# Kernel tuning notes

Measured on AMD Instinct MI355X. Metric: run time of the kernel, lower is better.

The kernel has to match this reference:

```python
import jax, jax.numpy as jnp
import numpy as np

DIM = 2048
N_HEADS = 32
N_KV_HEADS = 8
HEAD_DIM = 64
N_REP = N_HEADS // N_KV_HEADS
SEQ = 2048
BATCH = 1


def _llama3_scaled_rope(head_dim, end, base=10000.0, scale_factor=8):
    # matches executorch precompute_freqs_cis with use_scaled=True
    freqs = 1.0 / (base ** (np.arange(0, head_dim, 2)[: head_dim // 2] / head_dim))
    low_freq_factor, high_freq_factor, old_ctx = 1.0, 4.0, 8192.0
    low_wl = old_ctx / low_freq_factor
    high_wl = old_ctx / high_freq_factor
    wavelen = 2.0 * np.pi / freqs
    smooth = (old_ctx / wavelen - low_freq_factor) / (high_freq_factor - low_freq_factor)
    scaled = np.where(
        wavelen < high_wl,
        freqs,
        np.where(wavelen > low_wl, freqs / scale_factor,
                 (1.0 - smooth) * freqs / scale_factor + smooth * freqs),
    )
    t = np.arange(end, dtype=np.float64)
    ang = np.outer(t, scaled)
    return np.cos(ang).astype(np.float32), np.sin(ang).astype(np.float32)


def setup_inputs() -> dict:
    key = jax.random.key(0)
    kx, kq, kk, kv, ko = jax.random.split(key, 5)
    x = jax.random.normal(kx, (BATCH, SEQ, DIM), dtype=jnp.float32)
    sc = 0.02
    wq = jax.random.normal(kq, (N_HEADS * HEAD_DIM, DIM), dtype=jnp.float32) * sc
    wk = jax.random.normal(kk, (N_KV_HEADS * HEAD_DIM, DIM), dtype=jnp.float32) * sc
    wv = jax.random.normal(kv, (N_KV_HEADS * HEAD_DIM, DIM), dtype=jnp.float32) * sc
    wo = jax.random.normal(ko, (N_HEADS * HEAD_DIM, DIM), dtype=jnp.float32).T * sc
    cos, sin = _llama3_scaled_rope(HEAD_DIM, SEQ)
    return {"x": x, "freqs_cos": jnp.asarray(cos), "freqs_sin": jnp.asarray(sin),
            "wq": wq, "wk": wk, "wv": wv, "wo": wo}


def _apply_rotary(x, cos, sin):
    # x: [b, s, h, hd]; cos/sin: [s, hd//2]; interleaved-pair RoPE
    xr = x[..., 0::2]
    xi = x[..., 1::2]
    c = cos[None, :, None, :]
    s = sin[None, :, None, :]
    out_r = xr * c - xi * s
    out_i = xr * s + xi * c
    return jnp.stack([out_r, out_i], axis=-1).reshape(x.shape)


def reference(x, freqs_cos, freqs_sin, wq, wk, wv, wo):
    b, s, _ = x.shape
    q = (x @ wq.T).reshape(b, s, N_HEADS, HEAD_DIM)
    k = (x @ wk.T).reshape(b, s, N_KV_HEADS, HEAD_DIM)
    v = (x @ wv.T).reshape(b, s, N_KV_HEADS, HEAD_DIM)
    q = _apply_rotary(q, freqs_cos, freqs_sin)
    k = _apply_rotary(k, freqs_cos, freqs_sin)
    # [b, h, s, hd]
    q = q.transpose(0, 2, 1, 3)
    k = k.transpose(0, 2, 1, 3)
    v = v.transpose(0, 2, 1, 3)
    # GQA: repeat_interleave over head dim
    k = jnp.repeat(k, N_REP, axis=1)
    v = jnp.repeat(v, N_REP, axis=1)
    scale = 1.0 / jnp.sqrt(jnp.asarray(HEAD_DIM, dtype=x.dtype))
    scores = jnp.einsum("bhqd,bhkd->bhqk", q, k) * scale
    causal = jnp.tril(jnp.ones((s, s), dtype=bool))
    scores = jnp.where(causal[None, None], scores, jnp.finfo(scores.dtype).min)
    attn = jax.nn.softmax(scores, axis=-1)
    y = jnp.einsum("bhqk,bhkd->bhqd", attn, v)
    y = y.transpose(0, 2, 1, 3).reshape(b, s, N_HEADS * HEAD_DIM)
    return y @ wo.T
```

## Files before the change

kernel.cpp:

```cpp
#include <hip/hip_runtime.h>
#include <hip/hip_bf16.h>

typedef __attribute__((ext_vector_type(8))) __bf16 bf16x8;
typedef __attribute__((ext_vector_type(4))) __bf16 bf16x4;
typedef __attribute__((ext_vector_type(4))) float f32x4;

#define DIM 2048
#define SEQ 2048
#define NH 32
#define NKV 8
#define HD 64
#define QKVD 3072
#define KOFF 2048
#define VOFF 2560
#define KVDIM 512

__device__ __forceinline__ void gld16(const __bf16* g, __bf16* l) {
    __builtin_amdgcn_global_load_lds(
        (const __attribute__((address_space(1))) void*)g,
        (__attribute__((address_space(3))) void*)l, 16, 0, 0);
}

__global__ __launch_bounds__(256) void cvt_all(const float* __restrict__ x,
                                               const float* __restrict__ wq,
                                               const float* __restrict__ wk,
                                               const float* __restrict__ wv,
                                               const float* __restrict__ wo,
                                               __bf16* __restrict__ xb,
                                               __bf16* __restrict__ wqkvb,
                                               __bf16* __restrict__ wob) {
    const int i = blockIdx.x * blockDim.x + threadIdx.x;
    const int NX = SEQ * DIM / 4;
    const int NW = DIM * DIM / 4;
    const int NKV4 = KVDIM * DIM / 4;
    const float* src; __bf16* dst; int off;
    if (i < NX)                        { src = x;  dst = xb;    off = i; }
    else if (i < NX + NW)              { src = wq; dst = wqkvb; off = i - NX; }
    else if (i < NX + NW + NKV4)       { src = wk; dst = wqkvb + (size_t)KOFF * DIM; off = i - NX - NW; }
    else if (i < NX + NW + 2 * NKV4)   { src = wv; dst = wqkvb + (size_t)VOFF * DIM; off = i - NX - NW - NKV4; }
    else                               { src = wo; dst = wob;   off = i - NX - NW - 2 * NKV4; }
    float4 v = reinterpret_cast<const float4*>(src)[off];
    bf16x4 o;
    o[0] = (__bf16)v.x; o[1] = (__bf16)v.y; o[2] = (__bf16)v.z; o[3] = (__bf16)v.w;
    reinterpret_cast<bf16x4*>(dst)[off] = o;
}

template <typename OutT, bool ROPE>
__global__ __launch_bounds__(512, 6) void gemm_tn(const __bf16* __restrict__ A,
                                                  const __bf16* __restrict__ B,
                                                  OutT* __restrict__ C,
                                                  int M, int N, int K,
                                                  float scale, int scaleNlim,
                                                  const float* __restrict__ fc,
                                                  const float* __restrict__ fs,
                                                  __bf16* __restrict__ VTout) {
    __shared__ __align__(16) __bf16 As[2][2][128 * 32];
    __shared__ __align__(16) __bf16 Bs[2][2][64 * 32];
    const int tid = threadIdx.x;
    const int lane = tid & 63;
    const int w = tid >> 6;
    const int l15 = lane & 15, lhi = lane >> 4;
    const int mb = blockIdx.y * 128;
    const int nb = blockIdx.x * 64;
    const int wm = (w >> 1) * 32, wn = (w & 1) * 32;

    const int srow = lane >> 2, scol = (lane & 3) * 8;
    const __bf16* gA = A + (size_t)(mb + w * 16 + srow) * K + scol;
    const __bf16* gB = B + (size_t)(nb + (w & 3) * 16 + srow) * K + scol;
    const int bsub = w >> 2;

    auto stage = [&](int kk, int buf) {
#pragma unroll
        for (int s = 0; s < 2; ++s)
            gld16(gA + kk + s * 32, As[buf][s] + w * 512);
        gld16(gB + kk + bsub * 32, Bs[buf][bsub] + (w & 3) * 512);
    };

    stage(0, 0);
    __syncthreads();

    f32x4 acc[2][2] = {};
    int cur = 0;
    for (int kk = 0; kk < K; kk += 64, cur ^= 1) {
        if (kk + 64 < K) stage(kk + 64, cur ^ 1);
#pragma unroll
        for (int s = 0; s < 2; ++s) {
            bf16x8 a[2], b[2];
#pragma unroll
            for (int i = 0; i < 2; ++i)
                a[i] = *reinterpret_cast<const bf16x8*>(&As[cur][s][(wm + i * 16 + l15) * 32 + lhi * 8]);
#pragma unroll
            for (int j = 0; j < 2; ++j)
                b[j] = *reinterpret_cast<const bf16x8*>(&Bs[cur][s][(wn + j * 16 + l15) * 32 + lhi * 8]);
#pragma unroll
            for (int i = 0; i < 2; ++i)
#pragma unroll
                for (int j = 0; j < 2; ++j)
                    acc[i][j] = __builtin_amdgcn_mfma_f32_16x16x32_bf16(a[i], b[j], acc[i][j], 0, 0, 0);
        }
        __syncthreads();
    }

    const bool toVT = ROPE && (VTout != nullptr) && (nb >= VOFF);
    if (toVT) {
#pragma unroll
        for (int i = 0; i < 2; ++i)
#pragma unroll
            for (int j = 0; j < 2; ++j) {
                bf16x4 pv;
#pragma unroll
                for (int r = 0; r < 4; ++r) pv[r] = (__bf16)acc[i][j][r];
                const int colv = nb - VOFF + wn + j * 16 + l15;
                const int row0 = mb + wm + i * 16 + lhi * 4;
                *reinterpret_cast<bf16x4*>(VTout + (size_t)colv * M + row0) = pv;
            }
    } else {
        const float sc = (nb < scaleNlim) ? scale : 1.0f;
        const bool doRope = ROPE && (nb < VOFF);
#pragma unroll
        for (int i = 0; i < 2; ++i)
#pragma unroll
            for (int j = 0; j < 2; ++j)
#pragma unroll
                for (int r = 0; r < 4; ++r) {
                    float v = acc[i][j][r] * sc;
                    if (doRope) {
                        const int col = nb + wn + j * 16 + l15;
                        const int row = mb + wm + i * 16 + lhi * 4 + r;
                        const float vp = __shfl_xor(v, 1);
                        const int fi = (col & 63) >> 1;
                        const float cc = fc[row * 32 + fi];
                        const float ss = fs[row * 32 + fi];
                        v = (col & 1) ? (vp * ss + v * cc) : (v * cc - vp * ss);
                    }
                    C[(size_t)(mb + wm + i * 16 + lhi * 4 + r) * N + nb + wn + j * 16 + l15] = (OutT)v;
                }
    }
}

__global__ __launch_bounds__(256, 4) void attn_kernel(const __bf16* __restrict__ QKV,
                                                      const __bf16* __restrict__ VT,
                                                      __bf16* __restrict__ Y) {
    const int bx = blockIdx.x;
    const int g = bx >> 8;
    const int a = (bx >> 5) & 7;
    const int h = bx & 31;
    const int qt = (g == 0) ? 31 - a : (g == 1) ? a : (g == 2) ? 23 - a : 8 + a;
    const int kvh = h >> 2;
    const int tid = threadIdx.x;
    const int lane = tid & 63;
    const int w = tid >> 6;
    const int l15 = lane & 15, lhi = lane >> 4;

    __shared__ __align__(16) __bf16 Kl[2][64 * 64];
    __shared__ __align__(16) __bf16 Vl[2][64 * 64];
    __shared__ __align__(16) __bf16 Pl[4][16 * 64];

    const __bf16* Qp = QKV + h * HD;
    const __bf16* Kp = QKV + KOFF + kvh * HD;
    const __bf16* Vth = VT + (size_t)(kvh * HD) * SEQ;

    const int sr = lane >> 3;
    const int ksc = ((lane & 7) ^ sr) * 8;
    const int rswz = (l15 & 7);

    auto stage = [&](int jt, int buf) {
        const int kvb = jt * 64;
#pragma unroll
        for (int c = 0; c < 2; ++c) {
            const int row = w * 16 + c * 8;
            gld16(Kp + (size_t)(kvb + row + sr) * QKVD + ksc, &Kl[buf][row * 64]);
            gld16(Vth + (size_t)(row + sr) * SEQ + kvb + ksc, &Vl[buf][row * 64]);
        }
    };

    const int qb = qt * 64;
    const int qrow = qb + w * 16 + l15;

    const __bf16* qptr = Qp + (size_t)qrow * QKVD;
    bf16x8 qf0 = *reinterpret_cast<const bf16x8*>(qptr + lhi * 8);
    bf16x8 qf1 = *reinterpret_cast<const bf16x8*>(qptr + 32 + lhi * 8);

    f32x4 o[4] = {};
    float mrun = -1e30f;
    float lpart = 0.f;

    const int pkey = (l15 & 7) << 1;

    stage(0, 0);
    __syncthreads();

    int cur = 0;
    for (int j = 0; j <= qt; ++j, cur ^= 1) {
        const bool pre = (j < qt);
        if (pre) stage(j + 1, cur ^ 1);

        f32x4 sacc[4];
        __builtin_amdgcn_s_setprio(1);
#pragma unroll
        for (int t = 0; t < 4; ++t) {
            const int rb = (t * 16 + l15) * 64;
            bf16x8 kf0 = *reinterpret_cast<const bf16x8*>(
                &Kl[cur][rb + ((lhi ^ rswz) * 8)]);
            bf16x8 kf1 = *reinterpret_cast<const bf16x8*>(
                &Kl[cur][rb + (((4 + lhi) ^ rswz) * 8)]);
            f32x4 z = {0.f, 0.f, 0.f, 0.f};
            z = __builtin_amdgcn_mfma_f32_16x16x32_bf16(kf0, qf0, z, 0, 0, 0);
            z = __builtin_amdgcn_mfma_f32_16x16x32_bf16(kf1, qf1, z, 0, 0, 0);
            sacc[t] = z;
        }
        __builtin_amdgcn_s_setprio(0);

        if (j == qt) {
#pragma unroll
            for (int t = 0; t < 4; ++t)
#pragma unroll
                for (int r = 0; r < 4; ++r) {
                    const int kv = j * 64 + t * 16 + lhi * 4 + r;
                    if (kv > qrow) sacc[t][r] = -1e30f;
                }
        }

        float mt[4];
#pragma unroll
        for (int t = 0; t < 4; ++t)
            mt[t] = fmaxf(fmaxf(sacc[t][0], sacc[t][1]),
                          fmaxf(sacc[t][2], sacc[t][3]));
        const float pm = fmaxf(fmaxf(mt[0], mt[1]), fmaxf(mt[2], mt[3]));

        if (!__all(pm - mrun <= 8.0f)) {
            float full = pm;
            full = fmaxf(full, __shfl_xor(full, 16));
            full = fmaxf(full, __shfl_xor(full, 32));
            const float mn = fmaxf(mrun, full);
            const float aa = exp2f(mrun - mn);
            mrun = mn;
            lpart *= aa;
            float ar[4];
#pragma unroll
            for (int r = 0; r < 4; ++r) ar[r] = __shfl(aa, lhi * 4 + r);
#pragma unroll
            for (int t = 0; t < 4; ++t)
#pragma unroll
                for (int r = 0; r < 4; ++r) o[t][r] *= ar[r];
        }

#pragma unroll
        for (int t = 0; t < 4; ++t) {
            bf16x4 pk;
#pragma unroll
            for (int r = 0; r < 4; ++r) {
                const float pv = exp2f(sacc[t][r] - mrun);
                lpart += pv;
                pk[r] = (__bf16)pv;
            }
            const int sw = (t * 4 + lhi) ^ pkey;
            *reinterpret_cast<bf16x4*>(&Pl[w][l15 * 64 + sw * 4]) = pk;
        }

        bf16x8 pf0 = *reinterpret_cast<const bf16x8*>(
            &Pl[w][l15 * 64 + (((lhi * 2) ^ pkey) * 4)]);
        bf16x8 pf1 = *reinterpret_cast<const bf16x8*>(
            &Pl[w][l15 * 64 + (((8 + lhi * 2) ^ pkey) * 4)]);
        __builtin_amdgcn_s_setprio(1);
#pragma unroll
        for (int t = 0; t < 4; ++t) {
            const int rb = (t * 16 + l15) * 64;
            bf16x8 vf0 = *reinterpret_cast<const bf16x8*>(
                &Vl[cur][rb + ((lhi ^ rswz) * 8)]);
            bf16x8 vf1 = *reinterpret_cast<const bf16x8*>(
                &Vl[cur][rb + (((4 + lhi) ^ rswz) * 8)]);
            o[t] = __builtin_amdgcn_mfma_f32_16x16x32_bf16(pf0, vf0, o[t], 0, 0, 0);
            o[t] = __builtin_amdgcn_mfma_f32_16x16x32_bf16(pf1, vf1, o[t], 0, 0, 0);
        }
        __builtin_amdgcn_s_setprio(0);

        __syncthreads();
    }

    float ls = lpart;
    ls += __shfl_xor(ls, 16);
    ls += __shfl_xor(ls, 32);
    float lr[4];
#pragma unroll
    for (int r = 0; r < 4; ++r) lr[r] = __shfl(ls, lhi * 4 + r);
#pragma unroll
    for (int t = 0; t < 4; ++t)
#pragma unroll
        for (int r = 0; r < 4; ++r) {
            const float val = o[t][r] / lr[r];
            Y[(size_t)(qb + w * 16 + lhi * 4 + r) * DIM + h * HD + t * 16 + l15] =
                (__bf16)val;
        }
}

extern "C" void kernel_launch(void* const* d_in, const int* in_sizes, int n_in,
                              void* d_out, int out_size, void* d_ws, size_t ws_size,
                              hipStream_t stream) {
    const float* x    = (const float*)d_in[0];
    const float* fcos = (const float*)d_in[1];
    const float* fsin = (const float*)d_in[2];
    const float* wq   = (const float*)d_in[3];
    const float* wk   = (const float*)d_in[4];
    const float* wv   = (const float*)d_in[5];
    const float* wo   = (const float*)d_in[6];
    float* out = (float*)d_out;

    __bf16* xb    = (__bf16*)d_ws;
    __bf16* wqkvb = xb + (size_t)SEQ * DIM;
    __bf16* wob   = wqkvb + (size_t)QKVD * DIM;
    __bf16* QKVb  = wob + (size_t)DIM * DIM;
    __bf16* Yb    = QKVb + (size_t)SEQ * QKVD;
    __bf16* VTb   = Yb + (size_t)SEQ * DIM;

    const int ncvt = (SEQ * DIM / 4) + 2 * (DIM * DIM / 4) + 2 * (KVDIM * DIM / 4);
    cvt_all<<<ncvt / 256, 256, 0, stream>>>(x, wq, wk, wv, wo, xb, wqkvb, wob);

    gemm_tn<__bf16, true><<<dim3(QKVD / 64, SEQ / 128), 512, 0, stream>>>(
        xb, wqkvb, QKVb, SEQ, QKVD, DIM, 0.125f * 1.4426950408889634f, KOFF,
        fcos, fsin, VTb);

    attn_kernel<<<dim3(1024), 256, 0, stream>>>(QKVb, VTb, Yb);

    gemm_tn<float, false><<<dim3(DIM / 64, SEQ / 128), 512, 0, stream>>>(
        Yb, wob, out, SEQ, DIM, DIM, 1.0f, 0, nullptr, nullptr, nullptr);
}
```

Baseline: 132.0 us.

## Use 32x32 MFMA tiles with split-KV waves and merge partial softmax states

Rewrites the attention inner loop to use 32x32x16 bf16 MFMAs. Each wave now owns 32 query rows and half of the 64 keys in each KV tile, with the two KV halves combined at the end through an LDS exchange of running max, sum and partial outputs. The larger MFMA shape is meant to raise instruction efficiency and cut K/V LDS reads per FLOP. In exchange it adds a final cross-wave reduction and barrier, more accumulator registers, and idle waves on the diagonal tile.

```diff
diff --git a/kernel.cpp b/kernel.cpp
--- a/kernel.cpp
+++ b/kernel.cpp
@@ -4,6 +4,7 @@
 typedef __attribute__((ext_vector_type(8))) __bf16 bf16x8;
 typedef __attribute__((ext_vector_type(4))) __bf16 bf16x4;
 typedef __attribute__((ext_vector_type(4))) float f32x4;
+typedef __attribute__((ext_vector_type(16))) float f32x16;
 
 #define DIM 2048
 #define SEQ 2048
@@ -150,11 +151,15 @@
     const int tid = threadIdx.x;
     const int lane = tid & 63;
     const int w = tid >> 6;
-    const int l15 = lane & 15, lhi = lane >> 4;
-
-    __shared__ __align__(16) __bf16 Kl[2][64 * 64];
-    __shared__ __align__(16) __bf16 Vl[2][64 * 64];
-    __shared__ __align__(16) __bf16 Pl[4][16 * 64];
+    const int l31 = lane & 31;
+    const int lhi2 = lane >> 5;
+    const int qhalf = w & 1;
+    const int kvhalf = w >> 1;
+
+    __shared__ __align__(16) unsigned char smem[40960];
+    __bf16* Kl = (__bf16*)smem;
+    __bf16* Vl = (__bf16*)(smem + 16384);
+    __bf16* Pl = (__bf16*)(smem + 32768);
 
     const __bf16* Qp = QKV + h * HD;
     const __bf16* Kp = QKV + KOFF + kvh * HD;
@@ -162,30 +167,32 @@
 
     const int sr = lane >> 3;
     const int ksc = ((lane & 7) ^ sr) * 8;
-    const int rswz = (l15 & 7);
 
     auto stage = [&](int jt, int buf) {
         const int kvb = jt * 64;
 #pragma unroll
         for (int c = 0; c < 2; ++c) {
             const int row = w * 16 + c * 8;
-            gld16(Kp + (size_t)(kvb + row + sr) * QKVD + ksc, &Kl[buf][row * 64]);
-            gld16(Vth + (size_t)(row + sr) * SEQ + kvb + ksc, &Vl[buf][row * 64]);
+            gld16(Kp + (size_t)(kvb + row + sr) * QKVD + ksc, Kl + buf * 4096 + row * 64);
+            gld16(Vth + (size_t)(row + sr) * SEQ + kvb + ksc, Vl + buf * 4096 + row * 64);
         }
     };
 
     const int qb = qt * 64;
-    const int qrow = qb + w * 16 + l15;
+    const int qrow = qb + qhalf * 32 + l31;
 
     const __bf16* qptr = Qp + (size_t)qrow * QKVD;
-    bf16x8 qf0 = *reinterpret_cast<const bf16x8*>(qptr + lhi * 8);
-    bf16x8 qf1 = *reinterpret_cast<const bf16x8*>(qptr + 32 + lhi * 8);
-
-    f32x4 o[4] = {};
+    bf16x8 qf[4];
+#pragma unroll
+    for (int c = 0; c < 4; ++c)
+        qf[c] = *reinterpret_cast<const bf16x8*>(qptr + c * 16 + lhi2 * 8);
+
+    f32x16 o0 = {}, o1 = {};
     float mrun = -1e30f;
     float lpart = 0.f;
 
-    const int pkey = (l15 & 7) << 1;
+    const int pswz = l31 & 3;
+    const int rsw7 = l31 & 7;
 
     stage(0, 0);
     __syncthreads();
@@ -195,103 +202,116 @@
         const bool pre = (j < qt);
         if (pre) stage(j + 1, cur ^ 1);
 
-        f32x4 sacc[4];
-        __builtin_amdgcn_s_setprio(1);
-#pragma unroll
-        for (int t = 0; t < 4; ++t) {
-            const int rb = (t * 16 + l15) * 64;
-            bf16x8 kf0 = *reinterpret_cast<const bf16x8*>(
-                &Kl[cur][rb + ((lhi ^ rswz) * 8)]);
-            bf16x8 kf1 = *reinterpret_cast<const bf16x8*>(
-                &Kl[cur][rb + (((4 + lhi) ^ rswz) * 8)]);
-            f32x4 z = {0.f, 0.f, 0.f, 0.f};
-            z = __builtin_amdgcn_mfma_f32_16x16x32_bf16(kf0, qf0, z, 0, 0, 0);
-            z = __builtin_amdgcn_mfma_f32_16x16x32_bf16(kf1, qf1, z, 0, 0, 0);
-            sacc[t] = z;
-        }
-        __builtin_amdgcn_s_setprio(0);
-
-        if (j == qt) {
-#pragma unroll
-            for (int t = 0; t < 4; ++t)
-#pragma unroll
-                for (int r = 0; r < 4; ++r) {
-                    const int kv = j * 64 + t * 16 + lhi * 4 + r;
-                    if (kv > qrow) sacc[t][r] = -1e30f;
+        if (!(j == qt && kvhalf == 1 && qhalf == 0)) {
+            f32x16 sacc = {};
+            const __bf16* Kb = Kl + cur * 4096 + (kvhalf * 32 + l31) * 64;
+            __builtin_amdgcn_s_setprio(1);
+#pragma unroll
+            for (int c = 0; c < 4; ++c) {
+                bf16x8 kf = *reinterpret_cast<const bf16x8*>(
+                    Kb + (((c * 2 + lhi2) ^ rsw7) * 8));
+                sacc = __builtin_amdgcn_mfma_f32_32x32x16_bf16(kf, qf[c], sacc, 0, 0, 0);
+            }
+            __builtin_amdgcn_s_setprio(0);
+
+            if (j == qt && kvhalf == qhalf) {
+#pragma unroll
+                for (int r = 0; r < 16; ++r) {
+                    const int kvl = (r & 3) + 8 * (r >> 2) + 4 * lhi2;
+                    if (kvl > l31) sacc[r] = -1e30f;
                 }
-        }
-
-        float mt[4];
-#pragma unroll
-        for (int t = 0; t < 4; ++t)
-            mt[t] = fmaxf(fmaxf(sacc[t][0], sacc[t][1]),
-                          fmaxf(sacc[t][2], sacc[t][3]));
-        const float pm = fmaxf(fmaxf(mt[0], mt[1]), fmaxf(mt[2], mt[3]));
-
-        if (!__all(pm - mrun <= 8.0f)) {
-            float full = pm;
-            full = fmaxf(full, __shfl_xor(full, 16));
-            full = fmaxf(full, __shfl_xor(full, 32));
-            const float mn = fmaxf(mrun, full);
-            const float aa = exp2f(mrun - mn);
-            mrun = mn;
-            lpart *= aa;
-            float ar[4];
-#pragma unroll
-            for (int r = 0; r < 4; ++r) ar[r] = __shfl(aa, lhi * 4 + r);
-#pragma unroll
-            for (int t = 0; t < 4; ++t)
-#pragma unroll
-                for (int r = 0; r < 4; ++r) o[t][r] *= ar[r];
-        }
-
-#pragma unroll
-        for (int t = 0; t < 4; ++t) {
-            bf16x4 pk;
-#pragma unroll
-            for (int r = 0; r < 4; ++r) {
-                const float pv = exp2f(sacc[t][r] - mrun);
-                lpart += pv;
-                pk[r] = (__bf16)pv;
-            }
-            const int sw = (t * 4 + lhi) ^ pkey;
-            *reinterpret_cast<bf16x4*>(&Pl[w][l15 * 64 + sw * 4]) = pk;
-        }
-
-        bf16x8 pf0 = *reinterpret_cast<const bf16x8*>(
-            &Pl[w][l15 * 64 + (((lhi * 2) ^ pkey) * 4)]);
-        bf16x8 pf1 = *reinterpret_cast<const bf16x8*>(
-            &Pl[w][l15 * 64 + (((8 + lhi * 2) ^ pkey) * 4)]);
-        __builtin_amdgcn_s_setprio(1);
-#pragma unroll
-        for (int t = 0; t < 4; ++t) {
-            const int rb = (t * 16 + l15) * 64;
-            bf16x8 vf0 = *reinterpret_cast<const bf16x8*>(
-                &Vl[cur][rb + ((lhi ^ rswz) * 8)]);
-            bf16x8 vf1 = *reinterpret_cast<const bf16x8*>(
-                &Vl[cur][rb + (((4 + lhi) ^ rswz) * 8)]);
-            o[t] = __builtin_amdgcn_mfma_f32_16x16x32_bf16(pf0, vf0, o[t], 0, 0, 0);
-            o[t] = __builtin_amdgcn_mfma_f32_16x16x32_bf16(pf1, vf1, o[t], 0, 0, 0);
-        }
-        __builtin_amdgcn_s_setprio(0);
+            }
+
+            float pm = sacc[0];
+#pragma unroll
+            for (int r = 1; r < 16; ++r) pm = fmaxf(pm, sacc[r]);
+
+            if (!__all(pm - mrun <= 8.0f)) {
+                const float full = fmaxf(pm, __shfl_xor(pm, 32));
+                const float mn = fmaxf(mrun, full);
+                const float aa = exp2f(mrun - mn);
+                mrun = mn;
+                lpart *= aa;
+#pragma unroll
+                for (int r = 0; r < 16; ++r) {
+                    const int qi = (r & 3) + 8 * (r >> 2) + 4 * lhi2;
+                    const float ar = __shfl(aa, qi);
+                    o0[r] *= ar; o1[r] *= ar;
+                }
+            }
+
+            __bf16* Pw = Pl + w * 1024 + l31 * 32;
+            float ps = 0.f;
+#pragma unroll
+            for (int gg = 0; gg < 4; ++gg) {
+                bf16x4 pk;
+#pragma unroll
+                for (int rr = 0; rr < 4; ++rr) {
+                    const float pv = exp2f(sacc[gg * 4 + rr] - mrun);
+                    ps += pv;
+                    pk[rr] = (__bf16)pv;
+                }
+                *reinterpret_cast<bf16x4*>(Pw + ((gg ^ pswz) * 8) + lhi2 * 4) = pk;
+            }
+            lpart += ps;
+
+            bf16x8 pf[2];
+#pragma unroll
+            for (int c = 0; c < 2; ++c)
+                pf[c] = *reinterpret_cast<const bf16x8*>(
+                    Pw + (((c * 2 + lhi2) ^ pswz) * 8));
+            const __bf16* Vb0 = Vl + cur * 4096 + l31 * 64;
+            const __bf16* Vb1 = Vl + cur * 4096 + (32 + l31) * 64;
+            __builtin_amdgcn_s_setprio(1);
+#pragma unroll
+            for (int c = 0; c < 2; ++c) {
+                const int s = kvhalf * 4 + c * 2 + lhi2;
+                bf16x8 vf0 = *reinterpret_cast<const bf16x8*>(Vb0 + ((s ^ rsw7) * 8));
+                bf16x8 vf1 = *reinterpret_cast<const bf16x8*>(Vb1 + ((s ^ rsw7) * 8));
+                o0 = __builtin_amdgcn_mfma_f32_32x32x16_bf16(pf[c], vf0, o0, 0, 0, 0);
+                o1 = __builtin_amdgcn_mfma_f32_32x32x16_bf16(pf[c], vf1, o1, 0, 0, 0);
+            }
+            __builtin_amdgcn_s_setprio(0);
+        }
 
         __syncthreads();
     }
 
-    float ls = lpart;
-    ls += __shfl_xor(ls, 16);
-    ls += __shfl_xor(ls, 32);
-    float lr[4];
-#pragma unroll
-    for (int r = 0; r < 4; ++r) lr[r] = __shfl(ls, lhi * 4 + r);
-#pragma unroll
-    for (int t = 0; t < 4; ++t)
-#pragma unroll
-        for (int r = 0; r < 4; ++r) {
-            const float val = o[t][r] / lr[r];
-            Y[(size_t)(qb + w * 16 + lhi * 4 + r) * DIM + h * HD + t * 16 + l15] =
-                (__bf16)val;
-        }
+    const float ls = lpart + __shfl_xor(lpart, 32);
+    float* ex = (float*)smem;
+    float* exm = (float*)(smem + 32768);
+
+    if (kvhalf == 1) {
+        float* dst = ex + qhalf * 2048 + lane * 32;
+#pragma unroll
+        for (int r = 0; r < 16; ++r) { dst[r] = o0[r]; dst[16 + r] = o1[r]; }
+        if (lane < 32) {
+            exm[qhalf * 64 + l31] = mrun;
+            exm[qhalf * 64 + 32 + l31] = ls;
+        }
+    }
+    __syncthreads();
+    if (kvhalf == 0) {
+        const float mo = exm[qhalf * 64 + l31];
+        const float lso = exm[qhalf * 64 + 32 + l31];
+        const float mn = fmaxf(mrun, mo);
+        const float a0 = exp2f(mrun - mn);
+        const float a1 = exp2f(mo - mn);
+        const float lst = ls * a0 + lso * a1;
+        const float* src = ex + qhalf * 2048 + lane * 32;
+#pragma unroll
+        for (int r = 0; r < 16; ++r) {
+            const int qi = (r & 3) + 8 * (r >> 2) + 4 * lhi2;
+            const float A0 = __shfl(a0, qi);
+            const float A1 = __shfl(a1, qi);
+            const float L = __shfl(lst, qi);
+            const float v0 = (o0[r] * A0 + src[r] * A1) / L;
+            const float v1 = (o1[r] * A0 + src[16 + r] * A1) / L;
+            const size_t qg = (size_t)(qb + qhalf * 32 + qi);
+            Y[qg * DIM + h * HD + l31] = (__bf16)v0;
+            Y[qg * DIM + h * HD + 32 + l31] = (__bf16)v1;
+        }
+    }
 }
 
 extern "C" void kernel_launch(void* const* d_in, const int* in_sizes, int n_in,
```

Result: no change. 132.2 us (+0.2%).

## Load K/V fragments directly from global memory instead of LDS staging

Applied to the files above, without the earlier changes.

Removes the double-buffered LDS staging of K and V tiles in the attention kernel. Each wave now loads its own K and V MFMA fragments straight from global memory into registers every iteration, and the per-iteration block barrier is dropped. This avoids LDS traffic and synchronization, but each of the four waves fetches the same K/V data redundantly and there is no explicit prefetch, so load latency is exposed unless caches and other waves hide it.

```diff
diff --git a/kernel.cpp b/kernel.cpp
--- a/kernel.cpp
+++ b/kernel.cpp
@@ -152,28 +152,12 @@
     const int w = tid >> 6;
     const int l15 = lane & 15, lhi = lane >> 4;
 
-    __shared__ __align__(16) __bf16 Kl[2][64 * 64];
-    __shared__ __align__(16) __bf16 Vl[2][64 * 64];
     __shared__ __align__(16) __bf16 Pl[4][16 * 64];
 
     const __bf16* Qp = QKV + h * HD;
     const __bf16* Kp = QKV + KOFF + kvh * HD;
     const __bf16* Vth = VT + (size_t)(kvh * HD) * SEQ;
 
-    const int sr = lane >> 3;
-    const int ksc = ((lane & 7) ^ sr) * 8;
-    const int rswz = (l15 & 7);
-
-    auto stage = [&](int jt, int buf) {
-        const int kvb = jt * 64;
-#pragma unroll
-        for (int c = 0; c < 2; ++c) {
-            const int row = w * 16 + c * 8;
-            gld16(Kp + (size_t)(kvb + row + sr) * QKVD + ksc, &Kl[buf][row * 64]);
-            gld16(Vth + (size_t)(row + sr) * SEQ + kvb + ksc, &Vl[buf][row * 64]);
-        }
-    };
-
     const int qb = qt * 64;
     const int qrow = qb + w * 16 + l15;
 
@@ -181,32 +165,40 @@
     bf16x8 qf0 = *reinterpret_cast<const bf16x8*>(qptr + lhi * 8);
     bf16x8 qf1 = *reinterpret_cast<const bf16x8*>(qptr + 32 + lhi * 8);
 
+    const __bf16* Kb = Kp + (size_t)l15 * QKVD + lhi * 8;
+    const __bf16* Vb = Vth + (size_t)l15 * SEQ + lhi * 8;
+
     f32x4 o[4] = {};
     float mrun = -1e30f;
     float lpart = 0.f;
 
     const int pkey = (l15 & 7) << 1;
 
-    stage(0, 0);
-    __syncthreads();
-
-    int cur = 0;
-    for (int j = 0; j <= qt; ++j, cur ^= 1) {
-        const bool pre = (j < qt);
-        if (pre) stage(j + 1, cur ^ 1);
+    for (int j = 0; j <= qt; ++j) {
+        const int kvb = j * 64;
+
+        bf16x8 kf0[4], kf1[4];
+#pragma unroll
+        for (int t = 0; t < 4; ++t) {
+            const __bf16* kr = Kb + (size_t)(kvb + t * 16) * QKVD;
+            kf0[t] = *reinterpret_cast<const bf16x8*>(kr);
+            kf1[t] = *reinterpret_cast<const bf16x8*>(kr + 32);
+        }
+        bf16x8 vf0[4], vf1[4];
+#pragma unroll
+        for (int t = 0; t < 4; ++t) {
+            const __bf16* vr = Vb + (size_t)(t * 16) * SEQ + kvb;
+            vf0[t] = *reinterpret_cast<const bf16x8*>(vr);
+            vf1[t] = *reinterpret_cast<const bf16x8*>(vr + 32);
+        }
 
         f32x4 sacc[4];
         __builtin_amdgcn_s_setprio(1);
 #pragma unroll
         for (int t = 0; t < 4; ++t) {
-            const int rb = (t * 16 + l15) * 64;
-            bf16x8 kf0 = *reinterpret_cast<const bf16x8*>(
-                &Kl[cur][rb + ((lhi ^ rswz) * 8)]);
-            bf16x8 kf1 = *reinterpret_cast<const bf16x8*>(
-                &Kl[cur][rb + (((4 + lhi) ^ rswz) * 8)]);
             f32x4 z = {0.f, 0.f, 0.f, 0.f};
-            z = __builtin_amdgcn_mfma_f32_16x16x32_bf16(kf0, qf0, z, 0, 0, 0);
-            z = __builtin_amdgcn_mfma_f32_16x16x32_bf16(kf1, qf1, z, 0, 0, 0);
+            z = __builtin_amdgcn_mfma_f32_16x16x32_bf16(kf0[t], qf0, z, 0, 0, 0);
+            z = __builtin_amdgcn_mfma_f32_16x16x32_bf16(kf1[t], qf1, z, 0, 0, 0);
             sacc[t] = z;
         }
         __builtin_amdgcn_s_setprio(0);
@@ -216,7 +208,7 @@
             for (int t = 0; t < 4; ++t)
 #pragma unroll
                 for (int r = 0; r < 4; ++r) {
-                    const int kv = j * 64 + t * 16 + lhi * 4 + r;
+                    const int kv = kvb + t * 16 + lhi * 4 + r;
                     if (kv > qrow) sacc[t][r] = -1e30f;
                 }
         }
@@ -265,17 +257,10 @@
         __builtin_amdgcn_s_setprio(1);
 #pragma unroll
         for (int t = 0; t < 4; ++t) {
-            const int rb = (t * 16 + l15) * 64;
-            bf16x8 vf0 = *reinterpret_cast<const bf16x8*>(
-                &Vl[cur][rb + ((lhi ^ rswz) * 8)]);
-            bf16x8 vf1 = *reinterpret_cast<const bf16x8*>(
-                &Vl[cur][rb + (((4 + lhi) ^ rswz) * 8)]);
-            o[t] = __builtin_amdgcn_mfma_f32_16x16x32_bf16(pf0, vf0, o[t], 0, 0, 0);
-            o[t] = __builtin_amdgcn_mfma_f32_16x16x32_bf16(pf1, vf1, o[t], 0, 0, 0);
+            o[t] = __builtin_amdgcn_mfma_f32_16x16x32_bf16(pf0, vf0[t], o[t], 0, 0, 0);
+            o[t] = __builtin_amdgcn_mfma_f32_16x16x32_bf16(pf1, vf1[t], o[t], 0, 0, 0);
         }
         __builtin_amdgcn_s_setprio(0);
-
-        __syncthreads();
     }
 
     float ls = lpart;
```

After: 206.3 us. 1.56x slower.
